# Kernel tuning notes

Measured on AMD Instinct MI355X. Metric: run time of the kernel, lower is better.

The kernel has to match this reference:

```python
import jax, jax.numpy as jnp
import numpy as np

B, N, M, LDIM, RDIM, AGG = 4, 512, 512, 512, 512, 256


def setup_inputs() -> dict:
    key = jax.random.key(0)
    ks = jax.random.split(key, 7)
    data = jax.random.normal(ks[0], (B, N, LDIM), dtype=jnp.float32)
    crit = jax.random.normal(ks[1], (B, M, RDIM), dtype=jnp.float32)
    Wl = jax.random.normal(ks[2], (LDIM, AGG), dtype=jnp.float32) / np.sqrt(LDIM)
    bl = jax.random.normal(ks[3], (AGG,), dtype=jnp.float32) * 0.01
    Wr = jax.random.normal(ks[4], (RDIM, AGG), dtype=jnp.float32) / np.sqrt(RDIM)
    br = jax.random.normal(ks[5], (AGG,), dtype=jnp.float32) * 0.01
    agg = jax.random.uniform(ks[6], (AGG,), dtype=jnp.float32, minval=-0.01, maxval=0.01)
    return {"data": data, "crit": crit, "Wl": Wl, "bl": bl, "Wr": Wr, "br": br, "agg": agg}


def reference(data, crit, Wl, bl, Wr, br, agg):
    # linear projections
    datalin = jnp.einsum('bnl,la->bna', data, Wl) + bl   # [B,N,A]
    critlin = jnp.einsum('bmr,ra->bma', crit, Wr) + br   # [B,M,A]
    # broadcast add -> tanh -> reduce with agg vector: [B,N,M]
    linsum = jnp.tanh(datalin[:, :, None, :] + critlin[:, None, :, :])  # [B,N,M,A]
    dists = jnp.einsum('bnma,a->bnm', linsum, agg)
    return dists
```

## Files before the change

### kernel.cpp

```cpp
#include <hip/hip_runtime.h>


#define A_DIM 256
#define K_DIM 512
#define NROWS 2048

typedef unsigned short ushort;
typedef __attribute__((ext_vector_type(4))) unsigned short us4;
typedef __attribute__((ext_vector_type(8))) unsigned short us8;
typedef __attribute__((ext_vector_type(8))) short short8;
typedef __attribute__((ext_vector_type(4))) float f32x4;

__device__ inline ushort f2bf(float x) {
    union { float f; unsigned u; } v; v.f = x;
    unsigned r = v.u + 0x7FFFu + ((v.u >> 16) & 1u);
    return (ushort)(r >> 16);
}
__device__ inline float bf2f(ushort h) {
    union { unsigned u; float f; } v; v.u = ((unsigned)h) << 16; return v.f;
}
__device__ inline unsigned pack2bf(float lo, float hi) {
    return (unsigned)f2bf(lo) | ((unsigned)f2bf(hi) << 16);
}

__global__ __launch_bounds__(256) void transpose_w_kernel(
    const float* __restrict__ Wl, const float* __restrict__ Wr,
    ushort* __restrict__ wt)
{
    __shared__ float tile[64][68];
    const int t   = threadIdx.x;
    const int bid = blockIdx.x;
    const int at  = bid & 3;
    const int kt  = (bid >> 2) & 7;
    const int src = bid >> 5;
    const int a0 = at * 64, k0 = kt * 64;
    const float* W = src ? Wr : Wl;
    ushort* out = wt + (size_t)src * (A_DIM * K_DIM);

    const int c4 = (t & 15) * 4;
    const int kr = t >> 4;
#pragma unroll
    for (int r = 0; r < 4; r++) {
        const int k = kr + r * 16;
        *(float4*)&tile[k][c4] = *(const float4*)(W + (size_t)(k0 + k) * A_DIM + a0 + c4);
    }
    __syncthreads();
    const int aL  = t & 63;
    const int ks0 = (t >> 6) * 16;
#pragma unroll
    for (int g = 0; g < 4; g++) {
        us4 o;
#pragma unroll
        for (int i = 0; i < 4; i++) o[i] = f2bf(tile[ks0 + g * 4 + i][aL]);
        *(us4*)(out + (size_t)(a0 + aL) * K_DIM + k0 + ks0 + g * 4) = o;
    }
}

__global__ __launch_bounds__(256) void proj_mfma_kernel(
    const float* __restrict__ data, const float* __restrict__ crit,
    const float* __restrict__ bl, const float* __restrict__ br,
    const ushort* __restrict__ wt, ushort* __restrict__ eplanes)
{
    __shared__ ushort Ws[64][264];

    const int t   = threadIdx.x;
    const int bid = blockIdx.x;
    const int ct  = bid & 3;
    const int rt  = bid >> 2;
    const int src = rt >> 6;
    const int lr0 = (rt & 63) * 32;
    const int c0  = ct * 64;

    const float* X    = src ? crit : data;
    const float* bias = src ? br : bl;
    const ushort* Wt  = wt + (size_t)src * (A_DIM * K_DIM);
    ushort* E = eplanes + (size_t)src * ((size_t)A_DIM * NROWS);

    const int lane = t & 63;
    const int wid  = t >> 6;
    const int wm   = wid >> 1, wn = wid & 1;
    const int quad = lane >> 4, l16 = lane & 15;

    const float* xrow = X + (size_t)(lr0 + wm * 16 + l16) * K_DIM + quad * 8;
    const int aloc0 = wn * 32 + l16;

    f32x4 acc0 = {0.f, 0.f, 0.f, 0.f}, acc1 = {0.f, 0.f, 0.f, 0.f};

    float4 pa = *(const float4*)(xrow);
    float4 pb = *(const float4*)(xrow + 4);

    for (int kc = 0; kc < 2; kc++) {
        __syncthreads();
        {
            const int a  = t & 63;
            const int ks = (t >> 6) * 64;
            const ushort* s = Wt + (size_t)(c0 + a) * K_DIM + kc * 256 + ks;
#pragma unroll
            for (int i = 0; i < 8; i++)
                *(us8*)&Ws[a][ks + i * 8] = *(const us8*)(s + i * 8);
        }
        __syncthreads();

#pragma unroll
        for (int ls = 0; ls < 8; ls++) {
            const int s = kc * 8 + ls;
            float4 ca = pa, cb = pb;
            if (s < 15) {
                pa = *(const float4*)(xrow + (s + 1) * 32);
                pb = *(const float4*)(xrow + (s + 1) * 32 + 4);
            }
            union { short8 s8; unsigned u[4]; } af;
            af.u[0] = pack2bf(ca.x, ca.y);
            af.u[1] = pack2bf(ca.z, ca.w);
            af.u[2] = pack2bf(cb.x, cb.y);
            af.u[3] = pack2bf(cb.z, cb.w);
            short8 b0 = *(const short8*)&Ws[aloc0     ][ls * 32 + quad * 8];
            short8 b1 = *(const short8*)&Ws[aloc0 + 16][ls * 32 + quad * 8];
            acc0 = __builtin_amdgcn_mfma_f32_16x16x32_bf16(af.s8, b0, acc0, 0, 0, 0);
            acc1 = __builtin_amdgcn_mfma_f32_16x16x32_bf16(af.s8, b1, acc1, 0, 0, 0);
        }
    }

    const float c2 = 2.8853900817779268f;
    const int a_col0 = c0 + wn * 32 + l16;
    const int a_col1 = a_col0 + 16;
    const int row0   = lr0 + wm * 16 + quad * 4;
    const float bv0 = bias[a_col0], bv1 = bias[a_col1];
    us4 e0, e1;
#pragma unroll
    for (int i = 0; i < 4; i++) {
        float v0 = (acc0[i] + bv0) * c2;
        float v1 = (acc1[i] + bv1) * c2;
        v0 = fminf(fmaxf(v0, -15.f), 15.f);
        v1 = fminf(fmaxf(v1, -15.f), 15.f);
        e0[i] = f2bf(__builtin_amdgcn_exp2f(v0));
        e1[i] = f2bf(__builtin_amdgcn_exp2f(v1));
    }
    *(us4*)(E + (size_t)a_col0 * NROWS + row0) = e0;
    *(us4*)(E + (size_t)a_col1 * NROWS + row0) = e1;
}

__global__ __launch_bounds__(256) void tanh_reduce_kernel(
    const ushort* __restrict__ eplanes, const float* __restrict__ agg,
    float* __restrict__ partial)
{
    __shared__ __align__(16) float et [64][68];
    __shared__ __align__(16) float ect[64][68];
    __shared__ float aggs[128];

    const int t    = threadIdx.x;
    const int m0   = blockIdx.x * 64;
    const int n0   = blockIdx.y * 64;
    const int b    = blockIdx.z >> 1;
    const int half = blockIdx.z & 1;

    const size_t PLANE = (size_t)A_DIM * NROWS;
    const ushort* Ed = eplanes;
    const ushort* Ec = eplanes + PLANE;
    const int row_n = b * 512 + n0;
    const int row_m = b * 512 + m0;

    const int tx = t & 15;
    const int ty = t >> 4;

    if (t < 128) aggs[t] = 2.0f * agg[half * 128 + t];

    float acc[4][4];
#pragma unroll
    for (int i = 0; i < 4; i++)
#pragma unroll
        for (int j = 0; j < 4; j++) acc[i][j] = 0.f;
    float sagg = 0.f;

    const int aL = t >> 2;
    const int qd = t & 3;

    for (int ch = 0; ch < 2; ch++) {
        const int a0 = half * 128 + ch * 64;
        __syncthreads();
#pragma unroll
        for (int r = 0; r < 4; r++) {
            const int seg = qd * 16 + r * 4;
            us4 d = *(const us4*)(Ed + (size_t)(a0 + aL) * NROWS + row_n + seg);
            us4 c = *(const us4*)(Ec + (size_t)(a0 + aL) * NROWS + row_m + seg);
            float4 ev, cv;
            ev.x = bf2f(d[0]); ev.y = bf2f(d[1]); ev.z = bf2f(d[2]); ev.w = bf2f(d[3]);
            cv.x = bf2f(c[0]); cv.y = bf2f(c[1]); cv.z = bf2f(c[2]); cv.w = bf2f(c[3]);
            *(float4*)&et [aL][seg] = ev;
            *(float4*)&ect[aL][seg] = cv;
        }
        __syncthreads();

        for (int p = 0; p < 32; p++) {
            const float2 ag = *(const float2*)&aggs[ch * 64 + p * 2];
            sagg += ag.x + ag.y;
            float4 e0 = *(const float4*)&et [p * 2 + 0][ty * 4];
            float4 e1 = *(const float4*)&et [p * 2 + 1][ty * 4];
            float4 f0 = *(const float4*)&ect[p * 2 + 0][tx * 4];
            float4 f1 = *(const float4*)&ect[p * 2 + 1][tx * 4];
            const float ea0[4] = {e0.x, e0.y, e0.z, e0.w};
            const float ea1[4] = {e1.x, e1.y, e1.z, e1.w};
            const float fa0[4] = {f0.x, f0.y, f0.z, f0.w};
            const float fa1[4] = {f1.x, f1.y, f1.z, f1.w};
#pragma unroll
            for (int i = 0; i < 4; i++)
#pragma unroll
                for (int j = 0; j < 4; j++) {
                    float q0 = fmaf(ea0[i], fa0[j], 1.f);
                    float q1 = fmaf(ea1[i], fa1[j], 1.f);
                    acc[i][j] = fmaf(fmaf(ag.x, q1, ag.y * q0),
                                     __builtin_amdgcn_rcpf(q0 * q1), acc[i][j]);
                }
        }
    }

    const float base = 0.5f * sagg;
    float* pl = partial + (size_t)half * (1 << 20);
#pragma unroll
    for (int i = 0; i < 4; i++) {
        float4 v;
        v.x = base - acc[i][0]; v.y = base - acc[i][1];
        v.z = base - acc[i][2]; v.w = base - acc[i][3];
        *(float4*)(pl + ((size_t)(b * 512 + n0 + ty * 4 + i) * 512) + m0 + tx * 4) = v;
    }
}

__global__ __launch_bounds__(256) void combine_kernel(
    const float* __restrict__ partial, float* __restrict__ out)
{
    const int idx = blockIdx.x * 256 + threadIdx.x;
    const float4* p0 = (const float4*)partial;
    const float4* p1 = (const float4*)(partial + (1 << 20));
    float4* o = (float4*)out;
#pragma unroll
    for (int r = 0; r < 2; r++) {
        const int i = idx + r * 131072;
        float4 a = p0[i], b = p1[i], v;
        v.x = a.x + b.x; v.y = a.y + b.y; v.z = a.z + b.z; v.w = a.w + b.w;
        o[i] = v;
    }
}

extern "C" void kernel_launch(void* const* d_in, const int* in_sizes, int n_in,
                              void* d_out, int out_size, void* d_ws, size_t ws_size,
                              hipStream_t stream) {
    const float* data = (const float*)d_in[0];
    const float* crit = (const float*)d_in[1];
    const float* Wl   = (const float*)d_in[2];
    const float* bl   = (const float*)d_in[3];
    const float* Wr   = (const float*)d_in[4];
    const float* br   = (const float*)d_in[5];
    const float* agg  = (const float*)d_in[6];
    float* out = (float*)d_out;

    ushort* ws16 = (ushort*)d_ws;
    ushort* eplanes = ws16;
    ushort* wt      = ws16 + 2 * (size_t)A_DIM * NROWS;
    float* wspart   = (float*)((char*)d_ws + 8u * 1024u * 1024u);

    transpose_w_kernel<<<dim3(64), 256, 0, stream>>>(Wl, Wr, wt);

    proj_mfma_kernel<<<dim3(512), 256, 0, stream>>>(data, crit, bl, br, wt, eplanes);

    tanh_reduce_kernel<<<dim3(8, 8, 8), 256, 0, stream>>>(eplanes, agg, wspart);

    combine_kernel<<<dim3(512), 256, 0, stream>>>(wspart, out);
}
```

Baseline: 113.0 us.

## Fuse split-A partial combine into tanh-reduce via 512-thread blocks and LDS exchange

The two A-halves, previously computed by separate blocks writing partial buffers, now run as two 256-thread halves of one 512-thread block. The halves combine their results through shared memory before a single write to the output. This drops the separate combine kernel launch and the 8MB round-trip of partial results through global memory. In exchange the grid has half as many blocks, each using twice the LDS, which may lower occupancy.

Result: faster. 110.3 us (-2.4%).

```diff
diff --git a/kernel.cpp b/kernel.cpp
--- a/kernel.cpp
+++ b/kernel.cpp
@@ -140,19 +140,20 @@
     *(us4*)(E + (size_t)a_col1 * NROWS + row0) = e1;
 }
 
-__global__ __launch_bounds__(256) void tanh_reduce_kernel(
+__global__ __launch_bounds__(512) void tanh_reduce_kernel(
     const ushort* __restrict__ eplanes, const float* __restrict__ agg,
-    float* __restrict__ partial)
+    float* __restrict__ out)
 {
-    __shared__ __align__(16) float et [64][68];
-    __shared__ __align__(16) float ect[64][68];
-    __shared__ float aggs[128];
-
-    const int t    = threadIdx.x;
-    const int m0   = blockIdx.x * 64;
-    const int n0   = blockIdx.y * 64;
-    const int b    = blockIdx.z >> 1;
-    const int half = blockIdx.z & 1;
+    __shared__ __align__(16) float et [2][64][68];
+    __shared__ __align__(16) float ect[2][64][68];
+    __shared__ float aggs[256];
+
+    const int t  = threadIdx.x;
+    const int h  = t >> 8;
+    const int u  = t & 255;
+    const int m0 = blockIdx.x * 64;
+    const int n0 = blockIdx.y * 64;
+    const int b  = blockIdx.z;
 
     const size_t PLANE = (size_t)A_DIM * NROWS;
     const ushort* Ed = eplanes;
@@ -160,10 +161,10 @@
     const int row_n = b * 512 + n0;
     const int row_m = b * 512 + m0;
 
-    const int tx = t & 15;
-    const int ty = t >> 4;
-
-    if (t < 128) aggs[t] = 2.0f * agg[half * 128 + t];
+    const int tx = u & 15;
+    const int ty = u >> 4;
+
+    if (t < 256) aggs[t] = 2.0f * agg[t];
 
     float acc[4][4];
 #pragma unroll
@@ -172,11 +173,14 @@
         for (int j = 0; j < 4; j++) acc[i][j] = 0.f;
     float sagg = 0.f;
 
-    const int aL = t >> 2;
-    const int qd = t & 3;
+    const int aL = u >> 2;
+    const int qd = u & 3;
+
+    float (*eth)[68]  = et[h];
+    float (*ecth)[68] = ect[h];
 
     for (int ch = 0; ch < 2; ch++) {
-        const int a0 = half * 128 + ch * 64;
+        const int a0 = h * 128 + ch * 64;
         __syncthreads();
 #pragma unroll
         for (int r = 0; r < 4; r++) {
@@ -186,18 +190,18 @@
             float4 ev, cv;
             ev.x = bf2f(d[0]); ev.y = bf2f(d[1]); ev.z = bf2f(d[2]); ev.w = bf2f(d[3]);
             cv.x = bf2f(c[0]); cv.y = bf2f(c[1]); cv.z = bf2f(c[2]); cv.w = bf2f(c[3]);
-            *(float4*)&et [aL][seg] = ev;
-            *(float4*)&ect[aL][seg] = cv;
+            *(float4*)&eth [aL][seg] = ev;
+            *(float4*)&ecth[aL][seg] = cv;
         }
         __syncthreads();
 
         for (int p = 0; p < 32; p++) {
-            const float2 ag = *(const float2*)&aggs[ch * 64 + p * 2];
+            const float2 ag = *(const float2*)&aggs[h * 128 + ch * 64 + p * 2];
             sagg += ag.x + ag.y;
-            float4 e0 = *(const float4*)&et [p * 2 + 0][ty * 4];
-            float4 e1 = *(const float4*)&et [p * 2 + 1][ty * 4];
-            float4 f0 = *(const float4*)&ect[p * 2 + 0][tx * 4];
-            float4 f1 = *(const float4*)&ect[p * 2 + 1][tx * 4];
+            float4 e0 = *(const float4*)&eth [p * 2 + 0][ty * 4];
+            float4 e1 = *(const float4*)&eth [p * 2 + 1][ty * 4];
+            float4 f0 = *(const float4*)&ecth[p * 2 + 0][tx * 4];
+            float4 f1 = *(const float4*)&ecth[p * 2 + 1][tx * 4];
             const float ea0[4] = {e0.x, e0.y, e0.z, e0.w};
             const float ea1[4] = {e1.x, e1.y, e1.z, e1.w};
             const float fa0[4] = {f0.x, f0.y, f0.z, f0.w};
@@ -215,29 +219,26 @@
     }
 
     const float base = 0.5f * sagg;
-    float* pl = partial + (size_t)half * (1 << 20);
-#pragma unroll
-    for (int i = 0; i < 4; i++) {
-        float4 v;
-        v.x = base - acc[i][0]; v.y = base - acc[i][1];
-        v.z = base - acc[i][2]; v.w = base - acc[i][3];
-        *(float4*)(pl + ((size_t)(b * 512 + n0 + ty * 4 + i) * 512) + m0 + tx * 4) = v;
-    }
-}
-
-__global__ __launch_bounds__(256) void combine_kernel(
-    const float* __restrict__ partial, float* __restrict__ out)
-{
-    const int idx = blockIdx.x * 256 + threadIdx.x;
-    const float4* p0 = (const float4*)partial;
-    const float4* p1 = (const float4*)(partial + (1 << 20));
-    float4* o = (float4*)out;
-#pragma unroll
-    for (int r = 0; r < 2; r++) {
-        const int i = idx + r * 131072;
-        float4 a = p0[i], b = p1[i], v;
-        v.x = a.x + b.x; v.y = a.y + b.y; v.z = a.z + b.z; v.w = a.w + b.w;
-        o[i] = v;
+    float* xb = (float*)ect;
+    __syncthreads();
+    if (h == 1) {
+#pragma unroll
+        for (int i = 0; i < 4; i++)
+#pragma unroll
+            for (int j = 0; j < 4; j++)
+                xb[u * 17 + i * 4 + j] = base - acc[i][j];
+    }
+    __syncthreads();
+    if (h == 0) {
+#pragma unroll
+        for (int i = 0; i < 4; i++) {
+            float4 v;
+            v.x = (base - acc[i][0]) + xb[u * 17 + i * 4 + 0];
+            v.y = (base - acc[i][1]) + xb[u * 17 + i * 4 + 1];
+            v.z = (base - acc[i][2]) + xb[u * 17 + i * 4 + 2];
+            v.w = (base - acc[i][3]) + xb[u * 17 + i * 4 + 3];
+            *(float4*)(out + ((size_t)(b * 512 + n0 + ty * 4 + i) * 512) + m0 + tx * 4) = v;
+        }
     }
 }
 
@@ -256,13 +257,10 @@
     ushort* ws16 = (ushort*)d_ws;
     ushort* eplanes = ws16;
     ushort* wt      = ws16 + 2 * (size_t)A_DIM * NROWS;
-    float* wspart   = (float*)((char*)d_ws + 8u * 1024u * 1024u);
 
     transpose_w_kernel<<<dim3(64), 256, 0, stream>>>(Wl, Wr, wt);
 
     proj_mfma_kernel<<<dim3(512), 256, 0, stream>>>(data, crit, bl, br, wt, eplanes);
 
-    tanh_reduce_kernel<<<dim3(8, 8, 8), 256, 0, stream>>>(eplanes, agg, wspart);
-
-    combine_kernel<<<dim3(512), 256, 0, stream>>>(wspart, out);
-}
+    tanh_reduce_kernel<<<dim3(8, 8, 4), 512, 0, stream>>>(eplanes, agg, out);
+}
```
